# Kernel optimization log

Hardware: AMD Instinct MI355X
Metric: run time of the kernel (lower is better)

## Reference

```python
import jax, jax.numpy as jnp
import numpy as np

B, S, DIN, DOUT, E, K = 4, 2048, 1024, 1024, 16, 2


def setup_inputs() -> dict:
    key = jax.random.key(0)
    ks = jax.random.split(key, 6)
    sc = 1.0 / np.sqrt(DIN)
    return {
        "x": jax.random.normal(ks[0], (B, S, DIN), jnp.float32),
        "gate_w": jax.random.uniform(ks[1], (DIN, E), jnp.float32, -sc, sc),
        "gate_b": jax.random.uniform(ks[2], (E,), jnp.float32, -sc, sc),
        "expert_w": jax.random.uniform(ks[3], (E, DIN, DOUT), jnp.float32, -sc, sc),
        "expert_b": jax.random.uniform(ks[4], (E, DOUT), jnp.float32, -sc, sc),
        "expert_biases": jnp.zeros((E,), jnp.float32),
    }


def reference(x, gate_w, gate_b, expert_w, expert_b, expert_biases):
    # gating
    gate_output = x @ gate_w + gate_b                 # [B,S,E]
    gate_probs = jax.nn.sigmoid(gate_output)          # [B,S,E]
    gate_logits = gate_output + expert_biases         # bias-corrected routing logits
    _, top_k_idx = jax.lax.top_k(gate_logits, K)      # [B,S,K] int32
    top_k_probs = jnp.take_along_axis(gate_probs, top_k_idx, axis=-1)  # [B,S,K]
    top_k_probs = top_k_probs / top_k_probs.sum(-1, keepdims=True)

    # dense all-expert compute, as in the original torch.stack
    expert_outputs = jnp.einsum('bsd,edf->ebsf', x, expert_w) + expert_b[:, None, None, :]  # [E,B,S,DOUT]

    # Faithful replication of the torch gather (which, due to the permute,
    # reads channel j (0..K-1) of the selected expert and broadcasts it over DOUT):
    # out[d,b,s,j] = expert_outputs[topk[b,s,j], b, s, j]
    b_ix = jnp.arange(B)[:, None, None]
    s_ix = jnp.arange(S)[None, :, None]
    j_ix = jnp.arange(K)[None, None, :]
    gathered = expert_outputs[top_k_idx, b_ix, s_ix, j_ix]  # [B,S,K]

    final_scalar = (gathered * top_k_probs).sum(-1)          # [B,S]
    final_output = jnp.broadcast_to(final_scalar[..., None], (B, S, DOUT))
    return final_output, gate_probs, top_k_idx
```

## Files before the change

### kernel.cpp

```cpp
#include <hip/hip_runtime.h>
#include <math.h>
#include <float.h>

#define DIN_  1024
#define DOUT_ 1024
#define NE    16
#define KK    2
#define NTOK  8192


__global__ __launch_bounds__(256) void compact_w_kernel(
    const float* __restrict__ ew,
    float* __restrict__ wc)
{
    int i = blockIdx.x * 256 + threadIdx.x;
    if (i >= NE * KK * DIN_) return;
    int d = i & (DIN_ - 1);
    int j = (i >> 10) & 1;
    int e = i >> 11;
    wc[i] = ew[(size_t)e * DIN_ * DOUT_ + (size_t)d * DOUT_ + j];
}

__global__ __launch_bounds__(256) void moe_wave_kernel(
    const float* __restrict__ x,
    const float* __restrict__ gate_w,
    const float* __restrict__ gate_b,
    const float* __restrict__ ebias,
    const float* __restrict__ wc,
    const float* __restrict__ expert_b,
    float* __restrict__ out_final,
    float* __restrict__ out_probs,
    float* __restrict__ out_idx,
    int write_aux)
{
    const int lane = threadIdx.x & 63;
    const int wid  = threadIdx.x >> 6;
    const int tok0 = (blockIdx.x * 4 + wid) * 2;
    const int tok1 = tok0 + 1;

    const float4* x0p = (const float4*)(x + (size_t)tok0 * DIN_);
    const float4* x1p = (const float4*)(x + (size_t)tok1 * DIN_);
    float4 xr0[4], xr1[4];
#pragma unroll
    for (int c = 0; c < 4; c++) {
        xr0[c] = x0p[c * 64 + lane];
        xr1[c] = x1p[c * 64 + lane];
    }

    const float4* gw4 = (const float4*)gate_w;
    float a0[NE], a1[NE];
#pragma unroll
    for (int e = 0; e < NE; e++) { a0[e] = 0.f; a1[e] = 0.f; }

#pragma unroll
    for (int c = 0; c < 4; c++) {
#pragma unroll
        for (int j = 0; j < 4; j++) {
            int r = c * 256 + 4 * lane + j;
            float4 g0 = gw4[r * 4 + 0];
            float4 g1 = gw4[r * 4 + 1];
            float4 g2 = gw4[r * 4 + 2];
            float4 g3 = gw4[r * 4 + 3];
            float xs0 = (j == 0) ? xr0[c].x : (j == 1) ? xr0[c].y : (j == 2) ? xr0[c].z : xr0[c].w;
            float xs1 = (j == 0) ? xr1[c].x : (j == 1) ? xr1[c].y : (j == 2) ? xr1[c].z : xr1[c].w;
            a0[0]  += xs0 * g0.x; a0[1]  += xs0 * g0.y; a0[2]  += xs0 * g0.z; a0[3]  += xs0 * g0.w;
            a0[4]  += xs0 * g1.x; a0[5]  += xs0 * g1.y; a0[6]  += xs0 * g1.z; a0[7]  += xs0 * g1.w;
            a0[8]  += xs0 * g2.x; a0[9]  += xs0 * g2.y; a0[10] += xs0 * g2.z; a0[11] += xs0 * g2.w;
            a0[12] += xs0 * g3.x; a0[13] += xs0 * g3.y; a0[14] += xs0 * g3.z; a0[15] += xs0 * g3.w;
            a1[0]  += xs1 * g0.x; a1[1]  += xs1 * g0.y; a1[2]  += xs1 * g0.z; a1[3]  += xs1 * g0.w;
            a1[4]  += xs1 * g1.x; a1[5]  += xs1 * g1.y; a1[6]  += xs1 * g1.z; a1[7]  += xs1 * g1.w;
            a1[8]  += xs1 * g2.x; a1[9]  += xs1 * g2.y; a1[10] += xs1 * g2.z; a1[11] += xs1 * g2.w;
            a1[12] += xs1 * g3.x; a1[13] += xs1 * g3.y; a1[14] += xs1 * g3.z; a1[15] += xs1 * g3.w;
        }
    }

#pragma unroll
    for (int e = 0; e < NE; e++) {
        float v0 = a0[e], v1 = a1[e];
#pragma unroll
        for (int m = 32; m >= 1; m >>= 1) {
            v0 += __shfl_xor(v0, m, 64);
            v1 += __shfl_xor(v1, m, 64);
        }
        float gb = gate_b[e];
        a0[e] = v0 + gb;
        a1[e] = v1 + gb;
    }

    float eb[NE];
#pragma unroll
    for (int e = 0; e < NE; e++) eb[e] = ebias[e];

    int i00 = 0, i01 = 0, i10 = 0, i11 = 0;
    float w00, w01, w10, w11;
    {
        float best = a0[0] + eb[0], bgo = a0[0];
#pragma unroll
        for (int e = 1; e < NE; e++) {
            float lg = a0[e] + eb[e];
            if (lg > best) { best = lg; bgo = a0[e]; i00 = e; }
        }
        float best2 = -FLT_MAX, bgo2 = 0.f;
#pragma unroll
        for (int e = 0; e < NE; e++) {
            float lg = a0[e] + eb[e];
            bool c = (e != i00) && (lg > best2);
            if (c) { best2 = lg; bgo2 = a0[e]; i01 = e; }
        }
        float p0 = 1.f / (1.f + expf(-bgo));
        float p1 = 1.f / (1.f + expf(-bgo2));
        float inv = 1.f / (p0 + p1);
        w00 = p0 * inv; w01 = p1 * inv;
    }
    {
        float best = a1[0] + eb[0], bgo = a1[0];
#pragma unroll
        for (int e = 1; e < NE; e++) {
            float lg = a1[e] + eb[e];
            if (lg > best) { best = lg; bgo = a1[e]; i10 = e; }
        }
        float best2 = -FLT_MAX, bgo2 = 0.f;
#pragma unroll
        for (int e = 0; e < NE; e++) {
            float lg = a1[e] + eb[e];
            bool c = (e != i10) && (lg > best2);
            if (c) { best2 = lg; bgo2 = a1[e]; i11 = e; }
        }
        float p0 = 1.f / (1.f + expf(-bgo));
        float p1 = 1.f / (1.f + expf(-bgo2));
        float inv = 1.f / (p0 + p1);
        w10 = p0 * inv; w11 = p1 * inv;
    }

    if (write_aux) {
        int esel = lane & 15;
        float sg0 = 0.f, sg1 = 0.f;
#pragma unroll
        for (int e = 0; e < NE; e++) {
            bool m = (esel == e);
            sg0 = m ? a0[e] : sg0;
            sg1 = m ? a1[e] : sg1;
        }
        if (lane < 32) {
            int   t  = (lane < 16) ? tok0 : tok1;
            float sg = (lane < 16) ? sg0 : sg1;
            out_probs[(size_t)t * NE + esel] = 1.f / (1.f + expf(-sg));
        }
        if (lane == 0) {
            out_idx[(size_t)tok0 * KK + 0] = (float)i00;
            out_idx[(size_t)tok0 * KK + 1] = (float)i01;
        }
        if (lane == 1) {
            out_idx[(size_t)tok1 * KK + 0] = (float)i10;
            out_idx[(size_t)tok1 * KK + 1] = (float)i11;
        }
    }

    const float4* w0a = (const float4*)(wc + ((size_t)i00 * KK + 0) * DIN_);
    const float4* w0b = (const float4*)(wc + ((size_t)i01 * KK + 1) * DIN_);
    const float4* w1a = (const float4*)(wc + ((size_t)i10 * KK + 0) * DIN_);
    const float4* w1b = (const float4*)(wc + ((size_t)i11 * KK + 1) * DIN_);
    float d00 = 0.f, d01 = 0.f, d10 = 0.f, d11 = 0.f;
#pragma unroll
    for (int c = 0; c < 4; c++) {
        float4 p = w0a[c * 64 + lane];
        float4 q = w0b[c * 64 + lane];
        float4 u = w1a[c * 64 + lane];
        float4 v = w1b[c * 64 + lane];
        d00 += xr0[c].x * p.x + xr0[c].y * p.y + xr0[c].z * p.z + xr0[c].w * p.w;
        d01 += xr0[c].x * q.x + xr0[c].y * q.y + xr0[c].z * q.z + xr0[c].w * q.w;
        d10 += xr1[c].x * u.x + xr1[c].y * u.y + xr1[c].z * u.z + xr1[c].w * u.w;
        d11 += xr1[c].x * v.x + xr1[c].y * v.y + xr1[c].z * v.z + xr1[c].w * v.w;
    }
#pragma unroll
    for (int m = 32; m >= 1; m >>= 1) {
        d00 += __shfl_xor(d00, m, 64);
        d01 += __shfl_xor(d01, m, 64);
        d10 += __shfl_xor(d10, m, 64);
        d11 += __shfl_xor(d11, m, 64);
    }
    float f0 = w00 * (d00 + expert_b[(size_t)i00 * DOUT_ + 0])
             + w01 * (d01 + expert_b[(size_t)i01 * DOUT_ + 1]);
    float f1 = w10 * (d10 + expert_b[(size_t)i10 * DOUT_ + 0])
             + w11 * (d11 + expert_b[(size_t)i11 * DOUT_ + 1]);

    float4 f0v = make_float4(f0, f0, f0, f0);
    float4 f1v = make_float4(f1, f1, f1, f1);
    float4* o0 = (float4*)(out_final + (size_t)tok0 * DOUT_);
    float4* o1 = (float4*)(out_final + (size_t)tok1 * DOUT_);
#pragma unroll
    for (int c = 0; c < 4; c++) {
        o0[c * 64 + lane] = f0v;
        o1[c * 64 + lane] = f1v;
    }
}

extern "C" void kernel_launch(void* const* d_in, const int* in_sizes, int n_in,
                              void* d_out, int out_size, void* d_ws, size_t ws_size,
                              hipStream_t stream) {
    const float* x        = (const float*)d_in[0];
    const float* gate_w   = (const float*)d_in[1];
    const float* gate_b   = (const float*)d_in[2];
    const float* expert_w = (const float*)d_in[3];
    const float* expert_b = (const float*)d_in[4];
    const float* ebias    = (const float*)d_in[5];
    float* out = (float*)d_out;

    float* wc = (float*)d_ws;

    float* out_final = out;
    float* out_probs = out + (size_t)NTOK * DOUT_;
    float* out_idx   = out_probs + (size_t)NTOK * NE;
    int write_aux = (out_size >= NTOK * DOUT_ + NTOK * NE + NTOK * KK) ? 1 : 0;

    compact_w_kernel<<<(NE * KK * DIN_ + 255) / 256, 256, 0, stream>>>(expert_w, wc);
    moe_wave_kernel<<<NTOK / 8, 256, 0, stream>>>(
        x, gate_w, gate_b, ebias, wc, expert_b,
        out_final, out_probs, out_idx, write_aux);
}
```

Measured before the change: 159.5 us.

## Transpose gate weights and process four tokens per wave for gate reuse

The prep kernel now also writes a transposed copy of the gate weights ([E][DIN]), so each wave reads gate rows as coalesced float4 per expert. Each wave now handles four tokens instead of two, so every gate-weight load is reused across four tokens and the grid is halved. In exchange the kernel needs more registers (16 float4 of x plus 64 accumulators), which the launch-bounds hint tries to cap at 2 blocks per SIMD. There are also fewer waves to hide memory latency.

```diff
diff --git a/kernel.cpp b/kernel.cpp
--- a/kernel.cpp
+++ b/kernel.cpp
@@ -9,21 +9,29 @@
 #define NTOK  8192
 
 
-__global__ __launch_bounds__(256) void compact_w_kernel(
+__global__ __launch_bounds__(256) void prep_kernel(
     const float* __restrict__ ew,
-    float* __restrict__ wc)
+    const float* __restrict__ gw,
+    float* __restrict__ wc,
+    float* __restrict__ gwT)
 {
     int i = blockIdx.x * 256 + threadIdx.x;
-    if (i >= NE * KK * DIN_) return;
-    int d = i & (DIN_ - 1);
-    int j = (i >> 10) & 1;
-    int e = i >> 11;
-    wc[i] = ew[(size_t)e * DIN_ * DOUT_ + (size_t)d * DOUT_ + j];
+    if (i < NE * KK * DIN_) {
+        int d = i & (DIN_ - 1);
+        int j = (i >> 10) & 1;
+        int e = i >> 11;
+        wc[i] = ew[(size_t)e * DIN_ * DOUT_ + (size_t)d * DOUT_ + j];
+    } else if (i < NE * KK * DIN_ + NE * DIN_) {
+        int k = i - NE * KK * DIN_;
+        int d = k & (DIN_ - 1);
+        int e = k >> 10;
+        gwT[k] = gw[(size_t)d * NE + e];
+    }
 }
 
-__global__ __launch_bounds__(256) void moe_wave_kernel(
+__global__ __launch_bounds__(256, 2) void moe_wave_kernel(
     const float* __restrict__ x,
-    const float* __restrict__ gate_w,
+    const float* __restrict__ gwT,
     const float* __restrict__ gate_b,
     const float* __restrict__ ebias,
     const float* __restrict__ wc,
@@ -35,163 +43,130 @@
 {
     const int lane = threadIdx.x & 63;
     const int wid  = threadIdx.x >> 6;
-    const int tok0 = (blockIdx.x * 4 + wid) * 2;
-    const int tok1 = tok0 + 1;
+    const int tok0 = (blockIdx.x * 4 + wid) * 4;
 
-    const float4* x0p = (const float4*)(x + (size_t)tok0 * DIN_);
-    const float4* x1p = (const float4*)(x + (size_t)tok1 * DIN_);
-    float4 xr0[4], xr1[4];
+    float4 xr[4][4];
 #pragma unroll
-    for (int c = 0; c < 4; c++) {
-        xr0[c] = x0p[c * 64 + lane];
-        xr1[c] = x1p[c * 64 + lane];
+    for (int t = 0; t < 4; t++) {
+        const float4* xp = (const float4*)(x + (size_t)(tok0 + t) * DIN_);
+#pragma unroll
+        for (int c = 0; c < 4; c++) xr[t][c] = xp[c * 64 + lane];
     }
 
-    const float4* gw4 = (const float4*)gate_w;
-    float a0[NE], a1[NE];
+    const float4* gwT4 = (const float4*)gwT;
+    float acc[4][NE];
 #pragma unroll
-    for (int e = 0; e < NE; e++) { a0[e] = 0.f; a1[e] = 0.f; }
+    for (int t = 0; t < 4; t++)
+#pragma unroll
+        for (int e = 0; e < NE; e++) acc[t][e] = 0.f;
 
 #pragma unroll
-    for (int c = 0; c < 4; c++) {
+    for (int e = 0; e < NE; e++) {
+        float4 g[4];
 #pragma unroll
-        for (int j = 0; j < 4; j++) {
-            int r = c * 256 + 4 * lane + j;
-            float4 g0 = gw4[r * 4 + 0];
-            float4 g1 = gw4[r * 4 + 1];
-            float4 g2 = gw4[r * 4 + 2];
-            float4 g3 = gw4[r * 4 + 3];
-            float xs0 = (j == 0) ? xr0[c].x : (j == 1) ? xr0[c].y : (j == 2) ? xr0[c].z : xr0[c].w;
-            float xs1 = (j == 0) ? xr1[c].x : (j == 1) ? xr1[c].y : (j == 2) ? xr1[c].z : xr1[c].w;
-            a0[0]  += xs0 * g0.x; a0[1]  += xs0 * g0.y; a0[2]  += xs0 * g0.z; a0[3]  += xs0 * g0.w;
-            a0[4]  += xs0 * g1.x; a0[5]  += xs0 * g1.y; a0[6]  += xs0 * g1.z; a0[7]  += xs0 * g1.w;
-            a0[8]  += xs0 * g2.x; a0[9]  += xs0 * g2.y; a0[10] += xs0 * g2.z; a0[11] += xs0 * g2.w;
-            a0[12] += xs0 * g3.x; a0[13] += xs0 * g3.y; a0[14] += xs0 * g3.z; a0[15] += xs0 * g3.w;
-            a1[0]  += xs1 * g0.x; a1[1]  += xs1 * g0.y; a1[2]  += xs1 * g0.z; a1[3]  += xs1 * g0.w;
-            a1[4]  += xs1 * g1.x; a1[5]  += xs1 * g1.y; a1[6]  += xs1 * g1.z; a1[7]  += xs1 * g1.w;
-            a1[8]  += xs1 * g2.x; a1[9]  += xs1 * g2.y; a1[10] += xs1 * g2.z; a1[11] += xs1 * g2.w;
-            a1[12] += xs1 * g3.x; a1[13] += xs1 * g3.y; a1[14] += xs1 * g3.z; a1[15] += xs1 * g3.w;
+        for (int c = 0; c < 4; c++) g[c] = gwT4[e * 256 + c * 64 + lane];
+#pragma unroll
+        for (int t = 0; t < 4; t++) {
+#pragma unroll
+            for (int c = 0; c < 4; c++) {
+                acc[t][e] += xr[t][c].x * g[c].x + xr[t][c].y * g[c].y
+                           + xr[t][c].z * g[c].z + xr[t][c].w * g[c].w;
+            }
         }
     }
 
 #pragma unroll
     for (int e = 0; e < NE; e++) {
-        float v0 = a0[e], v1 = a1[e];
+        float gb = gate_b[e];
 #pragma unroll
-        for (int m = 32; m >= 1; m >>= 1) {
-            v0 += __shfl_xor(v0, m, 64);
-            v1 += __shfl_xor(v1, m, 64);
+        for (int t = 0; t < 4; t++) {
+            float v = acc[t][e];
+#pragma unroll
+            for (int m = 32; m >= 1; m >>= 1) v += __shfl_xor(v, m, 64);
+            acc[t][e] = v + gb;
         }
-        float gb = gate_b[e];
-        a0[e] = v0 + gb;
-        a1[e] = v1 + gb;
     }
 
     float eb[NE];
 #pragma unroll
     for (int e = 0; e < NE; e++) eb[e] = ebias[e];
 
-    int i00 = 0, i01 = 0, i10 = 0, i11 = 0;
-    float w00, w01, w10, w11;
-    {
-        float best = a0[0] + eb[0], bgo = a0[0];
+    int   i0[4], i1[4];
+    float w0[4], w1[4];
+#pragma unroll
+    for (int t = 0; t < 4; t++) {
+        int b0 = 0;
+        float best = acc[t][0] + eb[0], bgo = acc[t][0];
 #pragma unroll
         for (int e = 1; e < NE; e++) {
-            float lg = a0[e] + eb[e];
-            if (lg > best) { best = lg; bgo = a0[e]; i00 = e; }
+            float lg = acc[t][e] + eb[e];
+            if (lg > best) { best = lg; bgo = acc[t][e]; b0 = e; }
         }
+        int b1 = 0;
         float best2 = -FLT_MAX, bgo2 = 0.f;
 #pragma unroll
         for (int e = 0; e < NE; e++) {
-            float lg = a0[e] + eb[e];
-            bool c = (e != i00) && (lg > best2);
-            if (c) { best2 = lg; bgo2 = a0[e]; i01 = e; }
+            float lg = acc[t][e] + eb[e];
+            bool c = (e != b0) && (lg > best2);
+            if (c) { best2 = lg; bgo2 = acc[t][e]; b1 = e; }
         }
         float p0 = 1.f / (1.f + expf(-bgo));
         float p1 = 1.f / (1.f + expf(-bgo2));
         float inv = 1.f / (p0 + p1);
-        w00 = p0 * inv; w01 = p1 * inv;
-    }
-    {
-        float best = a1[0] + eb[0], bgo = a1[0];
-#pragma unroll
-        for (int e = 1; e < NE; e++) {
-            float lg = a1[e] + eb[e];
-            if (lg > best) { best = lg; bgo = a1[e]; i10 = e; }
-        }
-        float best2 = -FLT_MAX, bgo2 = 0.f;
-#pragma unroll
-        for (int e = 0; e < NE; e++) {
-            float lg = a1[e] + eb[e];
-            bool c = (e != i10) && (lg > best2);
-            if (c) { best2 = lg; bgo2 = a1[e]; i11 = e; }
-        }
-        float p0 = 1.f / (1.f + expf(-bgo));
-        float p1 = 1.f / (1.f + expf(-bgo2));
-        float inv = 1.f / (p0 + p1);
-        w10 = p0 * inv; w11 = p1 * inv;
+        i0[t] = b0; i1[t] = b1;
+        w0[t] = p0 * inv; w1[t] = p1 * inv;
     }
 
     if (write_aux) {
+        int tsel = lane >> 4;
         int esel = lane & 15;
-        float sg0 = 0.f, sg1 = 0.f;
+        float sg = 0.f;
 #pragma unroll
-        for (int e = 0; e < NE; e++) {
-            bool m = (esel == e);
-            sg0 = m ? a0[e] : sg0;
-            sg1 = m ? a1[e] : sg1;
-        }
-        if (lane < 32) {
-            int   t  = (lane < 16) ? tok0 : tok1;
-            float sg = (lane < 16) ? sg0 : sg1;
-            out_probs[(size_t)t * NE + esel] = 1.f / (1.f + expf(-sg));
-        }
-        if (lane == 0) {
-            out_idx[(size_t)tok0 * KK + 0] = (float)i00;
-            out_idx[(size_t)tok0 * KK + 1] = (float)i01;
-        }
-        if (lane == 1) {
-            out_idx[(size_t)tok1 * KK + 0] = (float)i10;
-            out_idx[(size_t)tok1 * KK + 1] = (float)i11;
+        for (int t = 0; t < 4; t++)
+#pragma unroll
+            for (int e = 0; e < NE; e++) {
+                bool m = (tsel == t) && (esel == e);
+                sg = m ? acc[t][e] : sg;
+            }
+        out_probs[(size_t)tok0 * NE + lane] = 1.f / (1.f + expf(-sg));
+        if (lane < 4) {
+            out_idx[(size_t)(tok0 + lane) * KK + 0] = (float)i0[lane];
+            out_idx[(size_t)(tok0 + lane) * KK + 1] = (float)i1[lane];
         }
     }
 
-    const float4* w0a = (const float4*)(wc + ((size_t)i00 * KK + 0) * DIN_);
-    const float4* w0b = (const float4*)(wc + ((size_t)i01 * KK + 1) * DIN_);
-    const float4* w1a = (const float4*)(wc + ((size_t)i10 * KK + 0) * DIN_);
-    const float4* w1b = (const float4*)(wc + ((size_t)i11 * KK + 1) * DIN_);
-    float d00 = 0.f, d01 = 0.f, d10 = 0.f, d11 = 0.f;
+    float d0[4], d1[4];
 #pragma unroll
-    for (int c = 0; c < 4; c++) {
-        float4 p = w0a[c * 64 + lane];
-        float4 q = w0b[c * 64 + lane];
-        float4 u = w1a[c * 64 + lane];
-        float4 v = w1b[c * 64 + lane];
-        d00 += xr0[c].x * p.x + xr0[c].y * p.y + xr0[c].z * p.z + xr0[c].w * p.w;
-        d01 += xr0[c].x * q.x + xr0[c].y * q.y + xr0[c].z * q.z + xr0[c].w * q.w;
-        d10 += xr1[c].x * u.x + xr1[c].y * u.y + xr1[c].z * u.z + xr1[c].w * u.w;
-        d11 += xr1[c].x * v.x + xr1[c].y * v.y + xr1[c].z * v.z + xr1[c].w * v.w;
+    for (int t = 0; t < 4; t++) {
+        const float4* wa = (const float4*)(wc + ((size_t)i0[t] * KK + 0) * DIN_);
+        const float4* wb = (const float4*)(wc + ((size_t)i1[t] * KK + 1) * DIN_);
+        float s0 = 0.f, s1 = 0.f;
+#pragma unroll
+        for (int c = 0; c < 4; c++) {
+            float4 p = wa[c * 64 + lane];
+            float4 q = wb[c * 64 + lane];
+            s0 += xr[t][c].x * p.x + xr[t][c].y * p.y + xr[t][c].z * p.z + xr[t][c].w * p.w;
+            s1 += xr[t][c].x * q.x + xr[t][c].y * q.y + xr[t][c].z * q.z + xr[t][c].w * q.w;
+        }
+        d0[t] = s0; d1[t] = s1;
     }
 #pragma unroll
     for (int m = 32; m >= 1; m >>= 1) {
-        d00 += __shfl_xor(d00, m, 64);
-        d01 += __shfl_xor(d01, m, 64);
-        d10 += __shfl_xor(d10, m, 64);
-        d11 += __shfl_xor(d11, m, 64);
+#pragma unroll
+        for (int t = 0; t < 4; t++) {
+            d0[t] += __shfl_xor(d0[t], m, 64);
+            d1[t] += __shfl_xor(d1[t], m, 64);
+        }
     }
-    float f0 = w00 * (d00 + expert_b[(size_t)i00 * DOUT_ + 0])
-             + w01 * (d01 + expert_b[(size_t)i01 * DOUT_ + 1]);
-    float f1 = w10 * (d10 + expert_b[(size_t)i10 * DOUT_ + 0])
-             + w11 * (d11 + expert_b[(size_t)i11 * DOUT_ + 1]);
 
-    float4 f0v = make_float4(f0, f0, f0, f0);
-    float4 f1v = make_float4(f1, f1, f1, f1);
-    float4* o0 = (float4*)(out_final + (size_t)tok0 * DOUT_);
-    float4* o1 = (float4*)(out_final + (size_t)tok1 * DOUT_);
 #pragma unroll
-    for (int c = 0; c < 4; c++) {
-        o0[c * 64 + lane] = f0v;
-        o1[c * 64 + lane] = f1v;
+    for (int t = 0; t < 4; t++) {
+        float f = w0[t] * (d0[t] + expert_b[(size_t)i0[t] * DOUT_ + 0])
+                + w1[t] * (d1[t] + expert_b[(size_t)i1[t] * DOUT_ + 1]);
+        float4 fv = make_float4(f, f, f, f);
+        float4* o = (float4*)(out_final + (size_t)(tok0 + t) * DOUT_);
+#pragma unroll
+        for (int c = 0; c < 4; c++) o[c * 64 + lane] = fv;
     }
 }
 
@@ -206,15 +181,17 @@
     const float* ebias    = (const float*)d_in[5];
     float* out = (float*)d_out;
 
-    float* wc = (float*)d_ws;
+    float* wc  = (float*)d_ws;
+    float* gwT = (float*)d_ws + (size_t)NE * KK * DIN_;
 
     float* out_final = out;
     float* out_probs = out + (size_t)NTOK * DOUT_;
     float* out_idx   = out_probs + (size_t)NTOK * NE;
     int write_aux = (out_size >= NTOK * DOUT_ + NTOK * NE + NTOK * KK) ? 1 : 0;
 
-    compact_w_kernel<<<(NE * KK * DIN_ + 255) / 256, 256, 0, stream>>>(expert_w, wc);
-    moe_wave_kernel<<<NTOK / 8, 256, 0, stream>>>(
-        x, gate_w, gate_b, ebias, wc, expert_b,
+    int prep_n = NE * KK * DIN_ + NE * DIN_;
+    prep_kernel<<<(prep_n + 255) / 256, 256, 0, stream>>>(expert_w, gate_w, wc, gwT);
+    moe_wave_kernel<<<NTOK / 16, 256, 0, stream>>>(
+        x, gwT, gate_b, ebias, wc, expert_b,
         out_final, out_probs, out_idx, write_aux);
 }
```

New measurement: 162.6 us. About the same (+2.0%).
